# Kernel optimization log

Hardware: AMD Instinct MI355X
Metric: run time of the kernel (lower is better)

Reference implementation:

```python
import jax, jax.numpy as jnp
import numpy as np

N_NODES = 50000
N_EDGES = 800000
IN_FEATS = 128
HIDDEN = 128
OUT_LEN = 128


def setup_inputs() -> dict:
    key = jax.random.key(0)
    ks = jax.random.split(key, 8)
    feat = jax.random.normal(ks[0], (N_NODES, IN_FEATS), dtype=jnp.float32)
    # Glorot-ish init for weights, zeros for bias (DGL GraphConv default)
    def w(k, fi, fo):
        return jax.random.normal(k, (fi, fo), dtype=jnp.float32) / np.sqrt(fi)
    W1 = w(ks[1], IN_FEATS, HIDDEN)
    W2 = w(ks[2], HIDDEN, HIDDEN)
    W3 = w(ks[3], HIDDEN, OUT_LEN)
    b1 = jnp.zeros((HIDDEN,), jnp.float32)
    b2 = jnp.zeros((HIDDEN,), jnp.float32)
    b3 = jnp.zeros((OUT_LEN,), jnp.float32)
    src = jax.random.randint(ks[4], (N_EDGES,), 0, N_NODES, dtype=jnp.int32)
    dst = jax.random.randint(ks[5], (N_EDGES,), 0, N_NODES, dtype=jnp.int32)
    return {"feat": feat, "W1": W1, "b1": b1, "W2": W2, "b2": b2,
            "W3": W3, "b3": b3, "src": src, "dst": dst}


def _degree_norm(idx, n):
    # degree counts, clamped to min 1 (DGL behavior), then ^{-1/2}
    deg = jax.ops.segment_sum(jnp.ones_like(idx, dtype=jnp.float32), idx,
                              num_segments=n)
    return jax.lax.rsqrt(jnp.maximum(deg, 1.0))


def _graph_conv(x, W, b, src, dst, out_norm, in_norm):
    # DGL GraphConv, norm='both':
    # h = D_dst^{-1/2} * segsum_dst( D_src^{-1/2} * x[src] ) @ W + b
    h = x * out_norm[:, None]
    m = jax.ops.segment_sum(h[src], dst, num_segments=x.shape[0])  # [N, d]
    m = m * in_norm[:, None]
    return m @ W + b


def reference(feat, W1, b1, W2, b2, W3, b3, src, dst):
    out_norm = _degree_norm(src, feat.shape[0])  # out-degree norm (source)
    in_norm = _degree_norm(dst, feat.shape[0])   # in-degree norm (dest)
    h = jax.nn.relu(_graph_conv(feat, W1, b1, src, dst, out_norm, in_norm))
    h = jax.nn.relu(_graph_conv(h, W2, b2, src, dst, out_norm, in_norm))
    h = _graph_conv(h, W3, b3, src, dst, out_norm, in_norm)
    # single graph: mean_nodes == mean over all nodes, then squeeze -> [out_len]
    return jnp.mean(h, axis=0)
```

## Files before the change

### kernel.cpp

```cpp
#include <hip/hip_runtime.h>

#define N_NODES 50000
#define N_EDGES 800000
#define F 128
#define SCAN_NB 49
#define RN_NB 196
#define CH 64
#define EPC (N_EDGES / CH)
#define HALF 25000
#define QTR 12500
#define BSTRIDE 17
#define AGG_NB (N_NODES / 4)
#define GB ((N_NODES + 63) / 64)

typedef __bf16 bf16x8 __attribute__((ext_vector_type(8)));
typedef float  f32x4  __attribute__((ext_vector_type(4)));
typedef float  f32x2  __attribute__((ext_vector_type(2)));

__device__ inline unsigned short f2bf(float f) {
    unsigned u = __float_as_uint(f);
    u += 0x7FFF + ((u >> 16) & 1);
    return (unsigned short)(u >> 16);
}
__device__ inline unsigned packbf2(float a, float b) {
    return (unsigned)f2bf(a) | ((unsigned)f2bf(b) << 16);
}

__device__ inline void fp8x8_to_f32(uint2 u, float* f) {
    f32x2 v0 = __builtin_amdgcn_cvt_pk_f32_fp8(u.x, false);
    f32x2 v1 = __builtin_amdgcn_cvt_pk_f32_fp8(u.x, true);
    f32x2 v2 = __builtin_amdgcn_cvt_pk_f32_fp8(u.y, false);
    f32x2 v3 = __builtin_amdgcn_cvt_pk_f32_fp8(u.y, true);
    f[0] = v0.x; f[1] = v0.y; f[2] = v1.x; f[3] = v1.y;
    f[4] = v2.x; f[5] = v2.y; f[6] = v3.x; f[7] = v3.y;
}
__device__ inline unsigned f32x4_to_fp8(float a, float b, float c, float d) {
    unsigned r = __builtin_amdgcn_cvt_pk_fp8_f32(a, b, 0, false);
    r = __builtin_amdgcn_cvt_pk_fp8_f32(c, d, r, true);
    return r;
}

__global__ __launch_bounds__(1024) void hist_kernel(const int* __restrict__ src,
                                                    const int* __restrict__ dst,
                                                    unsigned short* __restrict__ Hs16,
                                                    unsigned short* __restrict__ Hd16) {
    __shared__ unsigned hist[HALF / 2];
    int bx = blockIdx.x;
    int c = bx >> 2, t = bx & 1, h = (bx >> 1) & 1;
    const int* ids = t ? dst : src;
    unsigned short* H = t ? Hd16 : Hs16;
    int base = h * HALF;
    for (int j = threadIdx.x; j < HALF / 2; j += 1024) hist[j] = 0;
    __syncthreads();
    int e0 = c * EPC;
    for (int e = e0 + threadIdx.x; e < e0 + EPC; e += 1024) {
        int id = ids[e] - base;
        if ((unsigned)id < (unsigned)HALF)
            atomicAdd(&hist[id >> 1], 1u << ((id & 1) * 16));
    }
    __syncthreads();
    for (int j = threadIdx.x; j < HALF / 2; j += 1024)
        *(unsigned*)&H[(size_t)c * N_NODES + base + 2 * j] = hist[j];
}

__global__ __launch_bounds__(256) void reduceN_kernel(const unsigned short* __restrict__ Hs16,
                                                      const unsigned short* __restrict__ Hd16,
                                                      float* __restrict__ onorm,
                                                      float* __restrict__ inorm,
                                                      int* __restrict__ degd,
                                                      int* __restrict__ bsums) {
    __shared__ int wsum[4];
    int i = blockIdx.x * 256 + threadIdx.x;
    int dd = 0;
    if (i < N_NODES) {
        int ds = 0;
        for (int c = 0; c < CH; c++) {
            ds += Hs16[(size_t)c * N_NODES + i];
            dd += Hd16[(size_t)c * N_NODES + i];
        }
        onorm[i] = rsqrtf(fmaxf((float)ds, 1.0f));
        inorm[i] = rsqrtf(fmaxf((float)dd, 1.0f));
        degd[i] = dd;
    }
    int v = dd;
#pragma unroll
    for (int off = 32; off; off >>= 1) v += __shfl_down(v, off);
    if ((threadIdx.x & 63) == 0) wsum[threadIdx.x >> 6] = v;
    __syncthreads();
    if (threadIdx.x == 0)
        bsums[blockIdx.x] = wsum[0] + wsum[1] + wsum[2] + wsum[3];
}

__global__ __launch_bounds__(1024) void tq_kernel(const int* __restrict__ src,
                                                  const int* __restrict__ dst,
                                                  const float* __restrict__ inorm,
                                                  float* __restrict__ Tq,
                                                  const float* __restrict__ feat,
                                                  const float* __restrict__ onorm,
                                                  uint2* __restrict__ xq,
                                                  const float* __restrict__ W1,
                                                  const float* __restrict__ W2,
                                                  unsigned short* __restrict__ Wt) {
    __shared__ float a[QTR];
    int bx = blockIdx.x;
    int c = bx >> 2, q = bx & 3;
    int base = q * QTR;
    for (int j = threadIdx.x; j < QTR; j += 1024) a[j] = 0.0f;
    __syncthreads();
    int e0 = c * EPC;
    for (int e = e0 + threadIdx.x; e < e0 + EPC; e += 1024) {
        int s = src[e] - base;
        if ((unsigned)s < (unsigned)QTR)
            atomicAdd(&a[s], inorm[dst[e]]);
    }
    __syncthreads();
    for (int j = threadIdx.x; j < QTR; j += 1024)
        Tq[(size_t)c * N_NODES + base + j] = a[j];

    int T = gridDim.x * 1024;
    int id0 = bx * 1024 + threadIdx.x;
    for (int i = id0; i < N_NODES * F / 8; i += T) {
        float w = onorm[i >> 4];
        const float4* xv = (const float4*)feat;
        float4 v0 = xv[i * 2], v1 = xv[i * 2 + 1];
        uint2 o;
        o.x = f32x4_to_fp8(v0.x * w, v0.y * w, v0.z * w, v0.w * w);
        o.y = f32x4_to_fp8(v1.x * w, v1.y * w, v1.z * w, v1.w * w);
        xq[i] = o;
    }
    for (int i = id0; i < 2 * F * F; i += T) {
        int wi = i >> 14, rem = i & 16383;
        int n = rem >> 7, k = rem & 127;
        const float* W = wi ? W2 : W1;
        Wt[(size_t)wi * F * F + (size_t)n * F + k] = f2bf(W[k * F + n]);
    }
}

__global__ __launch_bounds__(1024) void scanC_kernel(const int* __restrict__ deg,
                                                     const int* __restrict__ bsums,
                                                     int* __restrict__ rowst,
                                                     const unsigned short* __restrict__ Hd16,
                                                     int* __restrict__ P,
                                                     const float* __restrict__ Tq,
                                                     float* __restrict__ qt) {
    __shared__ int wsum[16];
    int t = threadIdx.x, lane = t & 63, w = t >> 6;
    int i = blockIdx.x * 1024 + t;
    int v = (i < N_NODES) ? deg[i] : 0;
    int incl = v;
#pragma unroll
    for (int off = 1; off < 64; off <<= 1) {
        int u = __shfl_up(incl, off);
        if (lane >= off) incl += u;
    }
    if (lane == 63) wsum[w] = incl;
    __syncthreads();
    if (t == 0) {
        int s = 0;
        int kmax = min(4 * (int)blockIdx.x, RN_NB);
        for (int k = 0; k < kmax; k++) s += bsums[k];
#pragma unroll
        for (int k = 0; k < 16; k++) { int x = wsum[k]; wsum[k] = s; s += x; }
    }
    __syncthreads();
    incl += wsum[w];
    if (i < N_NODES) {
        int s = incl - v;
        rowst[i] = s;
        if (i == N_NODES - 1) rowst[N_NODES] = incl;
        float tsum = 0.0f;
        for (int c = 0; c < CH; c++) {
            size_t o = (size_t)c * N_NODES + i;
            P[o] = s; s += Hd16[o];
            tsum += Tq[o];
        }
        qt[i] = tsum;
    }
}

__global__ __launch_bounds__(1024) void scatter2_kernel(const int* __restrict__ src,
                                                        const int* __restrict__ dst,
                                                        const int* __restrict__ P,
                                                        int* __restrict__ esrc) {
    __shared__ int cur[QTR];
    int bx = blockIdx.x;
    int c = bx >> 2, q = bx & 3;
    int base = q * QTR;
    for (int j = threadIdx.x; j < QTR; j += 1024)
        cur[j] = P[(size_t)c * N_NODES + base + j];
    __syncthreads();
    int e0 = c * EPC;
    for (int e = e0 + threadIdx.x; e < e0 + EPC; e += 1024) {
        int d = dst[e] - base;
        if ((unsigned)d < (unsigned)QTR) {
            int pos = atomicAdd(&cur[d], 1);
            esrc[pos] = src[e];
        }
    }
}

__global__ __launch_bounds__(256) void agg_csr_kernel(const uint2* __restrict__ xq,
                                                      uint4* __restrict__ mb,
                                                      const int* __restrict__ rowst,
                                                      const int* __restrict__ esrc,
                                                      const float* __restrict__ inorm) {
    int w = threadIdx.x >> 6;
    int lane = threadIdx.x & 63;
    int g = lane >> 4, t = lane & 15;
    int row = blockIdx.x * 4 + w;
    int beg = __builtin_amdgcn_readfirstlane(rowst[row]);
    int end = __builtin_amdgcn_readfirstlane(rowst[row + 1]);
    float acc[8];
#pragma unroll
    for (int k = 0; k < 8; k++) acc[k] = 0.0f;

    for (int e = beg; e < end; e += 16) {
        int ea = min(e + g,      end - 1);
        int eb = min(e + 4 + g,  end - 1);
        int ec = min(e + 8 + g,  end - 1);
        int ed = min(e + 12 + g, end - 1);
        int sa = esrc[ea], sb = esrc[eb], sc = esrc[ec], sd = esrc[ed];
        uint2 ua = xq[(size_t)sa * 16 + t];
        uint2 ub = xq[(size_t)sb * 16 + t];
        uint2 uc = xq[(size_t)sc * 16 + t];
        uint2 ud = xq[(size_t)sd * 16 + t];
        float wa = (e + g      < end) ? 1.0f : 0.0f;
        float wb = (e + 4 + g  < end) ? 1.0f : 0.0f;
        float wc = (e + 8 + g  < end) ? 1.0f : 0.0f;
        float wd = (e + 12 + g < end) ? 1.0f : 0.0f;
        float fa[8], fb[8], fc[8], fd[8];
        fp8x8_to_f32(ua, fa); fp8x8_to_f32(ub, fb);
        fp8x8_to_f32(uc, fc); fp8x8_to_f32(ud, fd);
#pragma unroll
        for (int k = 0; k < 8; k++)
            acc[k] += fa[k] * wa + fb[k] * wb + fc[k] * wc + fd[k] * wd;
    }
#pragma unroll
    for (int k = 0; k < 8; k++) {
        acc[k] += __shfl_xor(acc[k], 16, 64);
        acc[k] += __shfl_xor(acc[k], 32, 64);
    }
    if (g == 0) {
        float inw = inorm[row];
        uint4 o;
        o.x = packbf2(acc[0] * inw, acc[1] * inw);
        o.y = packbf2(acc[2] * inw, acc[3] * inw);
        o.z = packbf2(acc[4] * inw, acc[5] * inw);
        o.w = packbf2(acc[6] * inw, acc[7] * inw);
        mb[(size_t)row * 16 + t] = o;
    }
}

template <int FINAL>
__global__ __launch_bounds__(256) void mfma_gemm_kernel(const unsigned short* __restrict__ A,
                                                        const unsigned short* __restrict__ Wt,
                                                        const float* __restrict__ bias,
                                                        const float* __restrict__ onorm,
                                                        unsigned char* __restrict__ Y8,
                                                        const float* __restrict__ qt,
                                                        float* __restrict__ part2) {
    __shared__ uint4 sB[F * BSTRIDE];
    __shared__ float sPf[4][F];
    int tid = threadIdx.x;
    int w = tid >> 6;
    int lane = tid & 63;
    int quad = lane >> 4, r16 = lane & 15;
    int row0 = blockIdx.x * 64 + w * 16;

    const uint4* Arow = (const uint4*)(A + (size_t)(row0 + r16) * F);
    uint4 a[4];
#pragma unroll
    for (int kk = 0; kk < 4; kk++) a[kk] = Arow[kk * 4 + quad];

    const uint4* G = (const uint4*)Wt;
    for (int j = tid; j < F * 16; j += 256)
        sB[(j >> 4) * BSTRIDE + (j & 15)] = G[j];

    f32x4 acc[8];
#pragma unroll
    for (int t = 0; t < 8; t++) acc[t] = (f32x4){0.f, 0.f, 0.f, 0.f};
    __syncthreads();

#pragma unroll
    for (int kk = 0; kk < 4; kk++) {
        bf16x8 av = __builtin_bit_cast(bf16x8, a[kk]);
#pragma unroll
        for (int t = 0; t < 8; t++) {
            bf16x8 bv = __builtin_bit_cast(bf16x8,
                sB[(t * 16 + r16) * BSTRIDE + kk * 4 + quad]);
            acc[t] = __builtin_amdgcn_mfma_f32_16x16x32_bf16(av, bv, acc[t], 0, 0, 0);
        }
    }

    float rw[4];
#pragma unroll
    for (int reg = 0; reg < 4; reg++) {
        int row = row0 + quad * 4 + reg;
        rw[reg] = (row < N_NODES) ? (FINAL ? qt[row] * onorm[row] : onorm[row]) : 0.0f;
    }

    if (!FINAL) {
#pragma unroll
        for (int t = 0; t < 8; t++) {
            int col = t * 16 + r16;
            float bb = bias[col];
#pragma unroll
            for (int reg = 0; reg < 4; reg++) {
                int row = row0 + quad * 4 + reg;
                if (row < N_NODES) {
                    float v = fmaxf(acc[t][reg] + bb, 0.0f) * rw[reg];
                    unsigned p = __builtin_amdgcn_cvt_pk_fp8_f32(v, v, 0, false);
                    Y8[(size_t)row * F + col] = (unsigned char)(p & 0xFF);
                }
            }
        }
    } else {
#pragma unroll
        for (int t = 0; t < 8; t++) {
            int col = t * 16 + r16;
            float bb = bias[col];
            float p = 0.0f;
#pragma unroll
            for (int reg = 0; reg < 4; reg++)
                p += fmaxf(acc[t][reg] + bb, 0.0f) * rw[reg];
            p += __shfl_xor(p, 16, 64);
            p += __shfl_xor(p, 32, 64);
            if (quad == 0) sPf[w][col] = p;
        }
        __syncthreads();
        if (tid < F)
            part2[(size_t)blockIdx.x * F + tid] =
                sPf[0][tid] + sPf[1][tid] + sPf[2][tid] + sPf[3][tid];
    }
}

__global__ __launch_bounds__(1024) void final_kernel(const float* __restrict__ part2,
                                                     const float* __restrict__ W3,
                                                     const float* __restrict__ b3,
                                                     float* __restrict__ out) {
    __shared__ float sc[8][F];
    int tid = threadIdx.x;
    int col = tid & 127, sl = tid >> 7;
    float acc = 0.0f;
    for (int b = sl; b < GB; b += 8) acc += part2[(size_t)b * F + col];
    sc[sl][col] = acc;
    __syncthreads();
    if (tid < F) {
        float s = 0.0f;
#pragma unroll
        for (int k = 0; k < 8; k++) s += sc[k][tid];
        sc[0][tid] = s * (1.0f / (float)N_NODES);
    }
    __syncthreads();
    if (tid < F) {
        float o = b3[tid];
        for (int k = 0; k < F; k++) o += sc[0][k] * W3[k * F + tid];
        out[tid] = o;
    }
}

extern "C" void kernel_launch(void* const* d_in, const int* in_sizes, int n_in,
                              void* d_out, int out_size, void* d_ws, size_t ws_size,
                              hipStream_t stream) {
    const float* feat = (const float*)d_in[0];
    const float* W1   = (const float*)d_in[1];
    const float* b1   = (const float*)d_in[2];
    const float* W2   = (const float*)d_in[3];
    const float* b2   = (const float*)d_in[4];
    const float* W3   = (const float*)d_in[5];
    const float* b3   = (const float*)d_in[6];
    const int*   src  = (const int*)d_in[7];
    const int*   dst  = (const int*)d_in[8];
    float* out = (float*)d_out;

    char* ws = (char*)d_ws;
    size_t off = 0;
    uint4* mb    = (uint4*)(ws + off); off += (size_t)N_NODES * F * 2;
    float* Tq    = (float*)(ws + off); off += (size_t)CH * N_NODES * 4;
    int*   P     = (int*)  (ws + off); off += (size_t)CH * N_NODES * 4;
    unsigned short* Hs16 = (unsigned short*)(ws + off); off += (size_t)CH * N_NODES * 2;
    unsigned short* Hd16 = (unsigned short*)(ws + off); off += (size_t)CH * N_NODES * 2;
    uint2* xq    = (uint2*)(ws + off); off += (size_t)N_NODES * F;
    uint2* hq    = (uint2*)(ws + off); off += (size_t)N_NODES * F;
    unsigned short* Wt = (unsigned short*)(ws + off); off += 2 * F * F * 2;
    float* part2 = (float*)(ws + off); off += (size_t)GB * F * 4;
    int*   esrc  = (int*)  (ws + off); off += (size_t)N_EDGES * 4;
    float* onorm = (float*)(ws + off); off += N_NODES * 4;
    float* inorm = (float*)(ws + off); off += N_NODES * 4;
    float* qt    = (float*)(ws + off); off += N_NODES * 4;
    int*   degd  = (int*)  (ws + off); off += N_NODES * 4;
    int*   rowst = (int*)  (ws + off); off += (N_NODES + 1) * 4;
    int*   bsums = (int*)  (ws + off); off += 256 * 4;

    hist_kernel<<<4 * CH, 1024, 0, stream>>>(src, dst, Hs16, Hd16);
    reduceN_kernel<<<RN_NB, 256, 0, stream>>>(Hs16, Hd16, onorm, inorm, degd, bsums);
    tq_kernel<<<4 * CH, 1024, 0, stream>>>(src, dst, inorm, Tq,
                                           feat, onorm, xq, W1, W2, Wt);
    scanC_kernel<<<SCAN_NB, 1024, 0, stream>>>(degd, bsums, rowst, Hd16, P, Tq, qt);
    scatter2_kernel<<<4 * CH, 1024, 0, stream>>>(src, dst, P, esrc);

    agg_csr_kernel<<<AGG_NB, 256, 0, stream>>>(xq, mb, rowst, esrc, inorm);
    mfma_gemm_kernel<0><<<GB, 256, 0, stream>>>((const unsigned short*)mb, Wt, b1,
                                                onorm, (unsigned char*)hq, qt, part2);
    agg_csr_kernel<<<AGG_NB, 256, 0, stream>>>(hq, mb, rowst, esrc, inorm);
    mfma_gemm_kernel<1><<<GB, 256, 0, stream>>>((const unsigned short*)mb, Wt + F * F,
                                                b2, onorm, (unsigned char*)hq, qt, part2);
    final_kernel<<<1, 1024, 0, stream>>>(part2, W3, b3, out);
}
```

Baseline: 233.0 us.

## Fuse CSR aggregation into MFMA GEMM kernel via shared-memory A tile

Merges the gather-aggregation kernel and the bf16 MFMA GEMM into one kernel. Each wave aggregates 16 destination rows one after another and stores the bf16 results in a shared-memory A tile, which the GEMM then consumes directly. This removes the intermediate mb buffer's global write and read and two kernel launches. In exchange, each wave now handles rows serially instead of one row per wave across many blocks, and the extra shared memory lowers occupancy. Both changes can cut the memory-level parallelism the latency-bound gather depends on.

Result: slower. 308.5 us (+32.4%).

```diff
diff --git a/kernel.cpp b/kernel.cpp
--- a/kernel.cpp
+++ b/kernel.cpp
@@ -10,7 +10,6 @@
 #define HALF 25000
 #define QTR 12500
 #define BSTRIDE 17
-#define AGG_NB (N_NODES / 4)
 #define GB ((N_NODES + 63) / 64)
 
 typedef __bf16 bf16x8 __attribute__((ext_vector_type(8)));
@@ -199,116 +198,110 @@
     }
 }
 
-__global__ __launch_bounds__(256) void agg_csr_kernel(const uint2* __restrict__ xq,
-                                                      uint4* __restrict__ mb,
-                                                      const int* __restrict__ rowst,
-                                                      const int* __restrict__ esrc,
-                                                      const float* __restrict__ inorm) {
-    int w = threadIdx.x >> 6;
-    int lane = threadIdx.x & 63;
-    int g = lane >> 4, t = lane & 15;
-    int row = blockIdx.x * 4 + w;
-    int beg = __builtin_amdgcn_readfirstlane(rowst[row]);
-    int end = __builtin_amdgcn_readfirstlane(rowst[row + 1]);
-    float acc[8];
-#pragma unroll
-    for (int k = 0; k < 8; k++) acc[k] = 0.0f;
-
-    for (int e = beg; e < end; e += 16) {
-        int ea = min(e + g,      end - 1);
-        int eb = min(e + 4 + g,  end - 1);
-        int ec = min(e + 8 + g,  end - 1);
-        int ed = min(e + 12 + g, end - 1);
-        int sa = esrc[ea], sb = esrc[eb], sc = esrc[ec], sd = esrc[ed];
-        uint2 ua = xq[(size_t)sa * 16 + t];
-        uint2 ub = xq[(size_t)sb * 16 + t];
-        uint2 uc = xq[(size_t)sc * 16 + t];
-        uint2 ud = xq[(size_t)sd * 16 + t];
-        float wa = (e + g      < end) ? 1.0f : 0.0f;
-        float wb = (e + 4 + g  < end) ? 1.0f : 0.0f;
-        float wc = (e + 8 + g  < end) ? 1.0f : 0.0f;
-        float wd = (e + 12 + g < end) ? 1.0f : 0.0f;
-        float fa[8], fb[8], fc[8], fd[8];
-        fp8x8_to_f32(ua, fa); fp8x8_to_f32(ub, fb);
-        fp8x8_to_f32(uc, fc); fp8x8_to_f32(ud, fd);
-#pragma unroll
-        for (int k = 0; k < 8; k++)
-            acc[k] += fa[k] * wa + fb[k] * wb + fc[k] * wc + fd[k] * wd;
-    }
-#pragma unroll
-    for (int k = 0; k < 8; k++) {
-        acc[k] += __shfl_xor(acc[k], 16, 64);
-        acc[k] += __shfl_xor(acc[k], 32, 64);
-    }
-    if (g == 0) {
-        float inw = inorm[row];
-        uint4 o;
-        o.x = packbf2(acc[0] * inw, acc[1] * inw);
-        o.y = packbf2(acc[2] * inw, acc[3] * inw);
-        o.z = packbf2(acc[4] * inw, acc[5] * inw);
-        o.w = packbf2(acc[6] * inw, acc[7] * inw);
-        mb[(size_t)row * 16 + t] = o;
-    }
-}
-
 template <int FINAL>
-__global__ __launch_bounds__(256) void mfma_gemm_kernel(const unsigned short* __restrict__ A,
-                                                        const unsigned short* __restrict__ Wt,
-                                                        const float* __restrict__ bias,
-                                                        const float* __restrict__ onorm,
-                                                        unsigned char* __restrict__ Y8,
-                                                        const float* __restrict__ qt,
-                                                        float* __restrict__ part2) {
+__global__ __launch_bounds__(256) void agg_gemm_kernel(const uint2* __restrict__ xq,
+                                                       const int* __restrict__ rowst,
+                                                       const int* __restrict__ esrc,
+                                                       const float* __restrict__ inorm,
+                                                       const unsigned short* __restrict__ Wt,
+                                                       const float* __restrict__ bias,
+                                                       const float* __restrict__ onorm,
+                                                       unsigned char* __restrict__ Y8,
+                                                       const float* __restrict__ qt,
+                                                       float* __restrict__ part2) {
     __shared__ uint4 sB[F * BSTRIDE];
+    __shared__ uint4 sA[64 * BSTRIDE];
     __shared__ float sPf[4][F];
     int tid = threadIdx.x;
     int w = tid >> 6;
     int lane = tid & 63;
     int quad = lane >> 4, r16 = lane & 15;
-    int row0 = blockIdx.x * 64 + w * 16;
-
-    const uint4* Arow = (const uint4*)(A + (size_t)(row0 + r16) * F);
-    uint4 a[4];
-#pragma unroll
-    for (int kk = 0; kk < 4; kk++) a[kk] = Arow[kk * 4 + quad];
+    int g = quad, t = r16;
+    int row0 = blockIdx.x * 64;
+    int rw0 = row0 + w * 16;
 
     const uint4* G = (const uint4*)Wt;
     for (int j = tid; j < F * 16; j += 256)
         sB[(j >> 4) * BSTRIDE + (j & 15)] = G[j];
 
+    for (int r = 0; r < 16; r++) {
+        int row = rw0 + r;
+        uint4 o = {0u, 0u, 0u, 0u};
+        if (row < N_NODES) {
+            int beg = __builtin_amdgcn_readfirstlane(rowst[row]);
+            int end = __builtin_amdgcn_readfirstlane(rowst[row + 1]);
+            float acc[8];
+#pragma unroll
+            for (int k = 0; k < 8; k++) acc[k] = 0.0f;
+            for (int e = beg; e < end; e += 16) {
+                int ea = min(e + g,      end - 1);
+                int eb = min(e + 4 + g,  end - 1);
+                int ec = min(e + 8 + g,  end - 1);
+                int ed = min(e + 12 + g, end - 1);
+                int sa = esrc[ea], sb = esrc[eb], sc = esrc[ec], sd = esrc[ed];
+                uint2 ua = xq[(size_t)sa * 16 + t];
+                uint2 ub = xq[(size_t)sb * 16 + t];
+                uint2 uc = xq[(size_t)sc * 16 + t];
+                uint2 ud = xq[(size_t)sd * 16 + t];
+                float wa = (e + g      < end) ? 1.0f : 0.0f;
+                float wb = (e + 4 + g  < end) ? 1.0f : 0.0f;
+                float wc = (e + 8 + g  < end) ? 1.0f : 0.0f;
+                float wd = (e + 12 + g < end) ? 1.0f : 0.0f;
+                float fa[8], fb[8], fc[8], fd[8];
+                fp8x8_to_f32(ua, fa); fp8x8_to_f32(ub, fb);
+                fp8x8_to_f32(uc, fc); fp8x8_to_f32(ud, fd);
+#pragma unroll
+                for (int k = 0; k < 8; k++)
+                    acc[k] += fa[k] * wa + fb[k] * wb + fc[k] * wc + fd[k] * wd;
+            }
+#pragma unroll
+            for (int k = 0; k < 8; k++) {
+                acc[k] += __shfl_xor(acc[k], 16, 64);
+                acc[k] += __shfl_xor(acc[k], 32, 64);
+            }
+            float inw = inorm[row];
+            o.x = packbf2(acc[0] * inw, acc[1] * inw);
+            o.y = packbf2(acc[2] * inw, acc[3] * inw);
+            o.z = packbf2(acc[4] * inw, acc[5] * inw);
+            o.w = packbf2(acc[6] * inw, acc[7] * inw);
+        }
+        if (g == 0) sA[(w * 16 + r) * BSTRIDE + t] = o;
+    }
+
     f32x4 acc[8];
 #pragma unroll
-    for (int t = 0; t < 8; t++) acc[t] = (f32x4){0.f, 0.f, 0.f, 0.f};
+    for (int n = 0; n < 8; n++) acc[n] = (f32x4){0.f, 0.f, 0.f, 0.f};
     __syncthreads();
 
 #pragma unroll
     for (int kk = 0; kk < 4; kk++) {
-        bf16x8 av = __builtin_bit_cast(bf16x8, a[kk]);
-#pragma unroll
-        for (int t = 0; t < 8; t++) {
+        bf16x8 av = __builtin_bit_cast(bf16x8,
+            sA[(w * 16 + r16) * BSTRIDE + kk * 4 + quad]);
+#pragma unroll
+        for (int n = 0; n < 8; n++) {
             bf16x8 bv = __builtin_bit_cast(bf16x8,
-                sB[(t * 16 + r16) * BSTRIDE + kk * 4 + quad]);
-            acc[t] = __builtin_amdgcn_mfma_f32_16x16x32_bf16(av, bv, acc[t], 0, 0, 0);
+                sB[(n * 16 + r16) * BSTRIDE + kk * 4 + quad]);
+            acc[n] = __builtin_amdgcn_mfma_f32_16x16x32_bf16(av, bv, acc[n], 0, 0, 0);
         }
     }
 
     float rw[4];
 #pragma unroll
     for (int reg = 0; reg < 4; reg++) {
-        int row = row0 + quad * 4 + reg;
+        int row = rw0 + quad * 4 + reg;
         rw[reg] = (row < N_NODES) ? (FINAL ? qt[row] * onorm[row] : onorm[row]) : 0.0f;
     }
 
     if (!FINAL) {
 #pragma unroll
-        for (int t = 0; t < 8; t++) {
-            int col = t * 16 + r16;
+        for (int n = 0; n < 8; n++) {
+            int col = n * 16 + r16;
             float bb = bias[col];
 #pragma unroll
             for (int reg = 0; reg < 4; reg++) {
-                int row = row0 + quad * 4 + reg;
+                int row = rw0 + quad * 4 + reg;
                 if (row < N_NODES) {
-                    float v = fmaxf(acc[t][reg] + bb, 0.0f) * rw[reg];
+                    float v = fmaxf(acc[n][reg] + bb, 0.0f) * rw[reg];
                     unsigned p = __builtin_amdgcn_cvt_pk_fp8_f32(v, v, 0, false);
                     Y8[(size_t)row * F + col] = (unsigned char)(p & 0xFF);
                 }
@@ -316,13 +309,13 @@
         }
     } else {
 #pragma unroll
-        for (int t = 0; t < 8; t++) {
-            int col = t * 16 + r16;
+        for (int n = 0; n < 8; n++) {
+            int col = n * 16 + r16;
             float bb = bias[col];
             float p = 0.0f;
 #pragma unroll
             for (int reg = 0; reg < 4; reg++)
-                p += fmaxf(acc[t][reg] + bb, 0.0f) * rw[reg];
+                p += fmaxf(acc[n][reg] + bb, 0.0f) * rw[reg];
             p += __shfl_xor(p, 16, 64);
             p += __shfl_xor(p, 32, 64);
             if (quad == 0) sPf[w][col] = p;
@@ -375,7 +368,6 @@
 
     char* ws = (char*)d_ws;
     size_t off = 0;
-    uint4* mb    = (uint4*)(ws + off); off += (size_t)N_NODES * F * 2;
     float* Tq    = (float*)(ws + off); off += (size_t)CH * N_NODES * 4;
     int*   P     = (int*)  (ws + off); off += (size_t)CH * N_NODES * 4;
     unsigned short* Hs16 = (unsigned short*)(ws + off); off += (size_t)CH * N_NODES * 2;
@@ -399,11 +391,9 @@
     scanC_kernel<<<SCAN_NB, 1024, 0, stream>>>(degd, bsums, rowst, Hd16, P, Tq, qt);
     scatter2_kernel<<<4 * CH, 1024, 0, stream>>>(src, dst, P, esrc);
 
-    agg_csr_kernel<<<AGG_NB, 256, 0, stream>>>(xq, mb, rowst, esrc, inorm);
-    mfma_gemm_kernel<0><<<GB, 256, 0, stream>>>((const unsigned short*)mb, Wt, b1,
-                                                onorm, (unsigned char*)hq, qt, part2);
-    agg_csr_kernel<<<AGG_NB, 256, 0, stream>>>(hq, mb, rowst, esrc, inorm);
-    mfma_gemm_kernel<1><<<GB, 256, 0, stream>>>((const unsigned short*)mb, Wt + F * F,
-                                                b2, onorm, (unsigned char*)hq, qt, part2);
+    agg_gemm_kernel<0><<<GB, 256, 0, stream>>>(xq, rowst, esrc, inorm, Wt, b1,
+                                               onorm, (unsigned char*)hq, qt, part2);
+    agg_gemm_kernel<1><<<GB, 256, 0, stream>>>(hq, rowst, esrc, inorm, Wt + F * F, b2,
+                                               onorm, (unsigned char*)hq, qt, part2);
     final_kernel<<<1, 1024, 0, stream>>>(part2, W3, b3, out);
 }
```

## Merge graph-preprocessing kernels into one cooperative kernel with grid syncs

Applied to the files above, without the earlier changes.

Replaces five separate preprocessing launches (histogram, degree reduce, Tq/quantize, scan, scatter) with a single cooperative kernel of 256 blocks of 1024 threads that separates the phases with grid.sync(). The goal is to remove the launch gaps and tail drain between the small phases. The degree-reduce step now runs on 49 blocks of 1024 threads instead of 196 blocks of 256, and the scan sums per-block totals accordingly. The risks are lower parallelism in those phases, the cost of each grid barrier, and the requirement that all 256 blocks be co-resident.

After: 381.7 us. +63.8%, slower.

```diff
diff --git a/kernel.cpp b/kernel.cpp
--- a/kernel.cpp
+++ b/kernel.cpp
@@ -1,10 +1,12 @@
 #include <hip/hip_runtime.h>
+#include <hip/hip_cooperative_groups.h>
+
+namespace cg = cooperative_groups;
 
 #define N_NODES 50000
 #define N_EDGES 800000
 #define F 128
 #define SCAN_NB 49
-#define RN_NB 196
 #define CH 64
 #define EPC (N_EDGES / CH)
 #define HALF 25000
@@ -40,161 +42,154 @@
     return r;
 }
 
-__global__ __launch_bounds__(1024) void hist_kernel(const int* __restrict__ src,
-                                                    const int* __restrict__ dst,
-                                                    unsigned short* __restrict__ Hs16,
-                                                    unsigned short* __restrict__ Hd16) {
-    __shared__ unsigned hist[HALF / 2];
+__global__ __launch_bounds__(1024) void build_kernel(
+        const int* __restrict__ src, const int* __restrict__ dst,
+        unsigned short* __restrict__ Hs16, unsigned short* __restrict__ Hd16,
+        float* __restrict__ onorm, float* __restrict__ inorm,
+        int* __restrict__ degd, int* __restrict__ bsums,
+        const float* __restrict__ feat, uint2* __restrict__ xq,
+        const float* __restrict__ W1, const float* __restrict__ W2,
+        unsigned short* __restrict__ Wt,
+        float* __restrict__ Tq, int* __restrict__ rowst,
+        int* __restrict__ P, float* __restrict__ qt,
+        int* __restrict__ esrc) {
+    cg::grid_group grid = cg::this_grid();
+    __shared__ __align__(16) unsigned ubuf[QTR];
+    __shared__ int wsum[16];
     int bx = blockIdx.x;
-    int c = bx >> 2, t = bx & 1, h = (bx >> 1) & 1;
-    const int* ids = t ? dst : src;
-    unsigned short* H = t ? Hd16 : Hs16;
-    int base = h * HALF;
-    for (int j = threadIdx.x; j < HALF / 2; j += 1024) hist[j] = 0;
-    __syncthreads();
-    int e0 = c * EPC;
-    for (int e = e0 + threadIdx.x; e < e0 + EPC; e += 1024) {
-        int id = ids[e] - base;
-        if ((unsigned)id < (unsigned)HALF)
-            atomicAdd(&hist[id >> 1], 1u << ((id & 1) * 16));
-    }
-    __syncthreads();
-    for (int j = threadIdx.x; j < HALF / 2; j += 1024)
-        *(unsigned*)&H[(size_t)c * N_NODES + base + 2 * j] = hist[j];
-}
-
-__global__ __launch_bounds__(256) void reduceN_kernel(const unsigned short* __restrict__ Hs16,
-                                                      const unsigned short* __restrict__ Hd16,
-                                                      float* __restrict__ onorm,
-                                                      float* __restrict__ inorm,
-                                                      int* __restrict__ degd,
-                                                      int* __restrict__ bsums) {
-    __shared__ int wsum[4];
-    int i = blockIdx.x * 256 + threadIdx.x;
-    int dd = 0;
-    if (i < N_NODES) {
-        int ds = 0;
-        for (int c = 0; c < CH; c++) {
-            ds += Hs16[(size_t)c * N_NODES + i];
-            dd += Hd16[(size_t)c * N_NODES + i];
-        }
-        onorm[i] = rsqrtf(fmaxf((float)ds, 1.0f));
-        inorm[i] = rsqrtf(fmaxf((float)dd, 1.0f));
-        degd[i] = dd;
-    }
-    int v = dd;
-#pragma unroll
-    for (int off = 32; off; off >>= 1) v += __shfl_down(v, off);
-    if ((threadIdx.x & 63) == 0) wsum[threadIdx.x >> 6] = v;
-    __syncthreads();
-    if (threadIdx.x == 0)
-        bsums[blockIdx.x] = wsum[0] + wsum[1] + wsum[2] + wsum[3];
-}
-
-__global__ __launch_bounds__(1024) void tq_kernel(const int* __restrict__ src,
-                                                  const int* __restrict__ dst,
-                                                  const float* __restrict__ inorm,
-                                                  float* __restrict__ Tq,
-                                                  const float* __restrict__ feat,
-                                                  const float* __restrict__ onorm,
-                                                  uint2* __restrict__ xq,
-                                                  const float* __restrict__ W1,
-                                                  const float* __restrict__ W2,
-                                                  unsigned short* __restrict__ Wt) {
-    __shared__ float a[QTR];
-    int bx = blockIdx.x;
-    int c = bx >> 2, q = bx & 3;
-    int base = q * QTR;
-    for (int j = threadIdx.x; j < QTR; j += 1024) a[j] = 0.0f;
-    __syncthreads();
-    int e0 = c * EPC;
-    for (int e = e0 + threadIdx.x; e < e0 + EPC; e += 1024) {
-        int s = src[e] - base;
-        if ((unsigned)s < (unsigned)QTR)
-            atomicAdd(&a[s], inorm[dst[e]]);
-    }
-    __syncthreads();
-    for (int j = threadIdx.x; j < QTR; j += 1024)
-        Tq[(size_t)c * N_NODES + base + j] = a[j];
-
-    int T = gridDim.x * 1024;
-    int id0 = bx * 1024 + threadIdx.x;
-    for (int i = id0; i < N_NODES * F / 8; i += T) {
-        float w = onorm[i >> 4];
-        const float4* xv = (const float4*)feat;
-        float4 v0 = xv[i * 2], v1 = xv[i * 2 + 1];
-        uint2 o;
-        o.x = f32x4_to_fp8(v0.x * w, v0.y * w, v0.z * w, v0.w * w);
-        o.y = f32x4_to_fp8(v1.x * w, v1.y * w, v1.z * w, v1.w * w);
-        xq[i] = o;
-    }
-    for (int i = id0; i < 2 * F * F; i += T) {
-        int wi = i >> 14, rem = i & 16383;
-        int n = rem >> 7, k = rem & 127;
-        const float* W = wi ? W2 : W1;
-        Wt[(size_t)wi * F * F + (size_t)n * F + k] = f2bf(W[k * F + n]);
-    }
-}
-
-__global__ __launch_bounds__(1024) void scanC_kernel(const int* __restrict__ deg,
-                                                     const int* __restrict__ bsums,
-                                                     int* __restrict__ rowst,
-                                                     const unsigned short* __restrict__ Hd16,
-                                                     int* __restrict__ P,
-                                                     const float* __restrict__ Tq,
-                                                     float* __restrict__ qt) {
-    __shared__ int wsum[16];
-    int t = threadIdx.x, lane = t & 63, w = t >> 6;
-    int i = blockIdx.x * 1024 + t;
-    int v = (i < N_NODES) ? deg[i] : 0;
-    int incl = v;
-#pragma unroll
-    for (int off = 1; off < 64; off <<= 1) {
-        int u = __shfl_up(incl, off);
-        if (lane >= off) incl += u;
-    }
-    if (lane == 63) wsum[w] = incl;
-    __syncthreads();
-    if (t == 0) {
-        int s = 0;
-        int kmax = min(4 * (int)blockIdx.x, RN_NB);
-        for (int k = 0; k < kmax; k++) s += bsums[k];
-#pragma unroll
-        for (int k = 0; k < 16; k++) { int x = wsum[k]; wsum[k] = s; s += x; }
-    }
-    __syncthreads();
-    incl += wsum[w];
-    if (i < N_NODES) {
-        int s = incl - v;
-        rowst[i] = s;
-        if (i == N_NODES - 1) rowst[N_NODES] = incl;
-        float tsum = 0.0f;
-        for (int c = 0; c < CH; c++) {
-            size_t o = (size_t)c * N_NODES + i;
-            P[o] = s; s += Hd16[o];
-            tsum += Tq[o];
-        }
-        qt[i] = tsum;
-    }
-}
-
-__global__ __launch_bounds__(1024) void scatter2_kernel(const int* __restrict__ src,
-                                                        const int* __restrict__ dst,
-                                                        const int* __restrict__ P,
-                                                        int* __restrict__ esrc) {
-    __shared__ int cur[QTR];
-    int bx = blockIdx.x;
-    int c = bx >> 2, q = bx & 3;
-    int base = q * QTR;
-    for (int j = threadIdx.x; j < QTR; j += 1024)
-        cur[j] = P[(size_t)c * N_NODES + base + j];
-    __syncthreads();
-    int e0 = c * EPC;
-    for (int e = e0 + threadIdx.x; e < e0 + EPC; e += 1024) {
-        int d = dst[e] - base;
-        if ((unsigned)d < (unsigned)QTR) {
-            int pos = atomicAdd(&cur[d], 1);
-            esrc[pos] = src[e];
+    int tid = threadIdx.x;
+
+    {
+        int c = bx >> 2, t = bx & 1, h = (bx >> 1) & 1;
+        const int* ids = t ? dst : src;
+        unsigned short* H = t ? Hd16 : Hs16;
+        int base = h * HALF;
+        for (int j = tid; j < HALF / 2; j += 1024) ubuf[j] = 0;
+        __syncthreads();
+        int e0 = c * EPC;
+        for (int e = e0 + tid; e < e0 + EPC; e += 1024) {
+            int id = ids[e] - base;
+            if ((unsigned)id < (unsigned)HALF)
+                atomicAdd(&ubuf[id >> 1], 1u << ((id & 1) * 16));
+        }
+        __syncthreads();
+        for (int j = tid; j < HALF / 2; j += 1024)
+            *(unsigned*)&H[(size_t)c * N_NODES + base + 2 * j] = ubuf[j];
+    }
+    grid.sync();
+
+    if (bx < SCAN_NB) {
+        int i = bx * 1024 + tid;
+        int dd = 0;
+        if (i < N_NODES) {
+            int ds = 0;
+            for (int c = 0; c < CH; c++) {
+                ds += Hs16[(size_t)c * N_NODES + i];
+                dd += Hd16[(size_t)c * N_NODES + i];
+            }
+            onorm[i] = rsqrtf(fmaxf((float)ds, 1.0f));
+            inorm[i] = rsqrtf(fmaxf((float)dd, 1.0f));
+            degd[i] = dd;
+        }
+        int v = dd;
+#pragma unroll
+        for (int off = 32; off; off >>= 1) v += __shfl_down(v, off);
+        if ((tid & 63) == 0) wsum[tid >> 6] = v;
+        __syncthreads();
+        if (tid == 0) {
+            int s = 0;
+#pragma unroll
+            for (int k = 0; k < 16; k++) s += wsum[k];
+            bsums[bx] = s;
+        }
+    }
+    grid.sync();
+
+    {
+        float* a = (float*)ubuf;
+        int c = bx >> 2, q = bx & 3;
+        int base = q * QTR;
+        for (int j = tid; j < QTR; j += 1024) a[j] = 0.0f;
+        __syncthreads();
+        int e0 = c * EPC;
+        for (int e = e0 + tid; e < e0 + EPC; e += 1024) {
+            int s = src[e] - base;
+            if ((unsigned)s < (unsigned)QTR)
+                atomicAdd(&a[s], inorm[dst[e]]);
+        }
+        __syncthreads();
+        for (int j = tid; j < QTR; j += 1024)
+            Tq[(size_t)c * N_NODES + base + j] = a[j];
+
+        int T = gridDim.x * 1024;
+        int id0 = bx * 1024 + tid;
+        for (int i = id0; i < N_NODES * F / 8; i += T) {
+            float w = onorm[i >> 4];
+            const float4* xv = (const float4*)feat;
+            float4 v0 = xv[i * 2], v1 = xv[i * 2 + 1];
+            uint2 o;
+            o.x = f32x4_to_fp8(v0.x * w, v0.y * w, v0.z * w, v0.w * w);
+            o.y = f32x4_to_fp8(v1.x * w, v1.y * w, v1.z * w, v1.w * w);
+            xq[i] = o;
+        }
+        for (int i = id0; i < 2 * F * F; i += T) {
+            int wi = i >> 14, rem = i & 16383;
+            int n = rem >> 7, k = rem & 127;
+            const float* W = wi ? W2 : W1;
+            Wt[(size_t)wi * F * F + (size_t)n * F + k] = f2bf(W[k * F + n]);
+        }
+    }
+    grid.sync();
+
+    if (bx < SCAN_NB) {
+        int t = tid, lane = t & 63, w = t >> 6;
+        int i = bx * 1024 + t;
+        int v = (i < N_NODES) ? degd[i] : 0;
+        int incl = v;
+#pragma unroll
+        for (int off = 1; off < 64; off <<= 1) {
+            int u = __shfl_up(incl, off);
+            if (lane >= off) incl += u;
+        }
+        if (lane == 63) wsum[w] = incl;
+        __syncthreads();
+        if (t == 0) {
+            int s = 0;
+            for (int k = 0; k < bx; k++) s += bsums[k];
+#pragma unroll
+            for (int k = 0; k < 16; k++) { int x = wsum[k]; wsum[k] = s; s += x; }
+        }
+        __syncthreads();
+        incl += wsum[w];
+        if (i < N_NODES) {
+            int s = incl - v;
+            rowst[i] = s;
+            if (i == N_NODES - 1) rowst[N_NODES] = incl;
+            float tsum = 0.0f;
+            for (int c = 0; c < CH; c++) {
+                size_t o = (size_t)c * N_NODES + i;
+                P[o] = s; s += Hd16[o];
+                tsum += Tq[o];
+            }
+            qt[i] = tsum;
+        }
+    }
+    grid.sync();
+
+    {
+        int* cur = (int*)ubuf;
+        int c = bx >> 2, q = bx & 3;
+        int base = q * QTR;
+        for (int j = tid; j < QTR; j += 1024)
+            cur[j] = P[(size_t)c * N_NODES + base + j];
+        __syncthreads();
+        int e0 = c * EPC;
+        for (int e = e0 + tid; e < e0 + EPC; e += 1024) {
+            int d = dst[e] - base;
+            if ((unsigned)d < (unsigned)QTR) {
+                int pos = atomicAdd(&cur[d], 1);
+                esrc[pos] = src[e];
+            }
         }
     }
 }
@@ -389,15 +384,18 @@
     float* inorm = (float*)(ws + off); off += N_NODES * 4;
     float* qt    = (float*)(ws + off); off += N_NODES * 4;
     int*   degd  = (int*)  (ws + off); off += N_NODES * 4;
-    int*   rowst = (int*)  (ws + off); off += (N_NODES + 1) * 4;
-    int*   bsums = (int*)  (ws + off); off += 256 * 4;
-
-    hist_kernel<<<4 * CH, 1024, 0, stream>>>(src, dst, Hs16, Hd16);
-    reduceN_kernel<<<RN_NB, 256, 0, stream>>>(Hs16, Hd16, onorm, inorm, degd, bsums);
-    tq_kernel<<<4 * CH, 1024, 0, stream>>>(src, dst, inorm, Tq,
-                                           feat, onorm, xq, W1, W2, Wt);
-    scanC_kernel<<<SCAN_NB, 1024, 0, stream>>>(degd, bsums, rowst, Hd16, P, Tq, qt);
-    scatter2_kernel<<<4 * CH, 1024, 0, stream>>>(src, dst, P, esrc);
+    int*   rowst = (int*)(ws + off); off += (N_NODES + 1) * 4;
+    int*   bsums = (int*)(ws + off); off += 256 * 4;
+
+    {
+        void* args[] = {(void*)&src, (void*)&dst, (void*)&Hs16, (void*)&Hd16,
+                        (void*)&onorm, (void*)&inorm, (void*)&degd, (void*)&bsums,
+                        (void*)&feat, (void*)&xq, (void*)&W1, (void*)&W2,
+                        (void*)&Wt, (void*)&Tq, (void*)&rowst, (void*)&P,
+                        (void*)&qt, (void*)&esrc};
+        hipLaunchCooperativeKernel((const void*)build_kernel, dim3(4 * CH),
+                                   dim3(1024), args, 0, stream);
+    }
 
     agg_csr_kernel<<<AGG_NB, 256, 0, stream>>>(xq, mb, rowst, esrc, inorm);
     mfma_gemm_kernel<0><<<GB, 256, 0, stream>>>((const unsigned short*)mb, Wt, b1,
```

## Replace chunked LDS histogram CSR build with global atomic degree and scatter

Applied to the files above, without the earlier changes.

Drops the 64-chunk shared-memory histograms, per-chunk prefix tables and the separate scatter pass. Degrees, the qt accumulation and CSR edge placement now use global atomics directly over vectorized int4 edge reads, with a simpler scan and an init kernel that zeroes buffers and transposes the weights. This removes large intermediate buffers (Hs16, Hd16, Tq, P) and the repeated edge passes, at the cost of contended global atomics and a nondeterministic edge order within rows. The GEMM row index is also clamped to avoid out-of-bounds reads on the last tile.

New measurement: 331.1 us. +42.1%, slower.

```diff
diff --git a/kernel.cpp b/kernel.cpp
--- a/kernel.cpp
+++ b/kernel.cpp
@@ -3,12 +3,8 @@
 #define N_NODES 50000
 #define N_EDGES 800000
 #define F 128
+#define RN_NB 196
 #define SCAN_NB 49
-#define RN_NB 196
-#define CH 64
-#define EPC (N_EDGES / CH)
-#define HALF 25000
-#define QTR 12500
 #define BSTRIDE 17
 #define AGG_NB (N_NODES / 4)
 #define GB ((N_NODES + 63) / 64)
@@ -40,47 +36,52 @@
     return r;
 }
 
-__global__ __launch_bounds__(1024) void hist_kernel(const int* __restrict__ src,
-                                                    const int* __restrict__ dst,
-                                                    unsigned short* __restrict__ Hs16,
-                                                    unsigned short* __restrict__ Hd16) {
-    __shared__ unsigned hist[HALF / 2];
-    int bx = blockIdx.x;
-    int c = bx >> 2, t = bx & 1, h = (bx >> 1) & 1;
-    const int* ids = t ? dst : src;
-    unsigned short* H = t ? Hd16 : Hs16;
-    int base = h * HALF;
-    for (int j = threadIdx.x; j < HALF / 2; j += 1024) hist[j] = 0;
-    __syncthreads();
-    int e0 = c * EPC;
-    for (int e = e0 + threadIdx.x; e < e0 + EPC; e += 1024) {
-        int id = ids[e] - base;
-        if ((unsigned)id < (unsigned)HALF)
-            atomicAdd(&hist[id >> 1], 1u << ((id & 1) * 16));
-    }
-    __syncthreads();
-    for (int j = threadIdx.x; j < HALF / 2; j += 1024)
-        *(unsigned*)&H[(size_t)c * N_NODES + base + 2 * j] = hist[j];
-}
-
-__global__ __launch_bounds__(256) void reduceN_kernel(const unsigned short* __restrict__ Hs16,
-                                                      const unsigned short* __restrict__ Hd16,
-                                                      float* __restrict__ onorm,
-                                                      float* __restrict__ inorm,
-                                                      int* __restrict__ degd,
-                                                      int* __restrict__ bsums) {
+__global__ __launch_bounds__(256) void init_kernel(int* __restrict__ degS,
+                                                   int* __restrict__ degD,
+                                                   float* __restrict__ qtacc,
+                                                   const float* __restrict__ W1,
+                                                   const float* __restrict__ W2,
+                                                   unsigned short* __restrict__ Wt) {
+    int T = gridDim.x * 256;
+    int id0 = blockIdx.x * 256 + threadIdx.x;
+    for (int i = id0; i < N_NODES; i += T) {
+        degS[i] = 0; degD[i] = 0; qtacc[i] = 0.0f;
+    }
+    for (int i = id0; i < 2 * F * F; i += T) {
+        int wi = i >> 14, rem = i & 16383;
+        int n = rem >> 7, k = rem & 127;
+        const float* W = wi ? W2 : W1;
+        Wt[(size_t)wi * F * F + (size_t)n * F + k] = f2bf(W[k * F + n]);
+    }
+}
+
+__global__ __launch_bounds__(1024) void deg_kernel(const int4* __restrict__ src4,
+                                                   const int4* __restrict__ dst4,
+                                                   int* __restrict__ degS,
+                                                   int* __restrict__ degD) {
+    int T = gridDim.x * 1024;
+    for (int i = blockIdx.x * 1024 + threadIdx.x; i < N_EDGES / 4; i += T) {
+        int4 s = src4[i], d = dst4[i];
+        atomicAdd(&degS[s.x], 1); atomicAdd(&degS[s.y], 1);
+        atomicAdd(&degS[s.z], 1); atomicAdd(&degS[s.w], 1);
+        atomicAdd(&degD[d.x], 1); atomicAdd(&degD[d.y], 1);
+        atomicAdd(&degD[d.z], 1); atomicAdd(&degD[d.w], 1);
+    }
+}
+
+__global__ __launch_bounds__(256) void norms_kernel(const int* __restrict__ degS,
+                                                    const int* __restrict__ degD,
+                                                    float* __restrict__ onorm,
+                                                    float* __restrict__ inorm,
+                                                    int* __restrict__ bsums) {
     __shared__ int wsum[4];
     int i = blockIdx.x * 256 + threadIdx.x;
     int dd = 0;
     if (i < N_NODES) {
-        int ds = 0;
-        for (int c = 0; c < CH; c++) {
-            ds += Hs16[(size_t)c * N_NODES + i];
-            dd += Hd16[(size_t)c * N_NODES + i];
-        }
+        int ds = degS[i];
+        dd = degD[i];
         onorm[i] = rsqrtf(fmaxf((float)ds, 1.0f));
         inorm[i] = rsqrtf(fmaxf((float)dd, 1.0f));
-        degd[i] = dd;
     }
     int v = dd;
 #pragma unroll
@@ -91,34 +92,68 @@
         bsums[blockIdx.x] = wsum[0] + wsum[1] + wsum[2] + wsum[3];
 }
 
-__global__ __launch_bounds__(1024) void tq_kernel(const int* __restrict__ src,
-                                                  const int* __restrict__ dst,
-                                                  const float* __restrict__ inorm,
-                                                  float* __restrict__ Tq,
-                                                  const float* __restrict__ feat,
-                                                  const float* __restrict__ onorm,
-                                                  uint2* __restrict__ xq,
-                                                  const float* __restrict__ W1,
-                                                  const float* __restrict__ W2,
-                                                  unsigned short* __restrict__ Wt) {
-    __shared__ float a[QTR];
-    int bx = blockIdx.x;
-    int c = bx >> 2, q = bx & 3;
-    int base = q * QTR;
-    for (int j = threadIdx.x; j < QTR; j += 1024) a[j] = 0.0f;
-    __syncthreads();
-    int e0 = c * EPC;
-    for (int e = e0 + threadIdx.x; e < e0 + EPC; e += 1024) {
-        int s = src[e] - base;
-        if ((unsigned)s < (unsigned)QTR)
-            atomicAdd(&a[s], inorm[dst[e]]);
-    }
-    __syncthreads();
-    for (int j = threadIdx.x; j < QTR; j += 1024)
-        Tq[(size_t)c * N_NODES + base + j] = a[j];
-
+__global__ __launch_bounds__(1024) void scan_kernel(const int* __restrict__ degD,
+                                                    const int* __restrict__ bsums,
+                                                    int* __restrict__ rowst,
+                                                    int* __restrict__ cur) {
+    __shared__ int wsum[16];
+    __shared__ int sbase;
+    int t = threadIdx.x, lane = t & 63, w = t >> 6;
+    int i = blockIdx.x * 1024 + t;
+    int v = (i < N_NODES) ? degD[i] : 0;
+    int incl = v;
+#pragma unroll
+    for (int off = 1; off < 64; off <<= 1) {
+        int u = __shfl_up(incl, off);
+        if (lane >= off) incl += u;
+    }
+    if (lane == 63) wsum[w] = incl;
+    int kmax = min(4 * (int)blockIdx.x, RN_NB);
+    if (t < 64) {
+        int s = 0;
+        for (int k = t; k < kmax; k += 64) s += bsums[k];
+#pragma unroll
+        for (int off = 32; off; off >>= 1) s += __shfl_down(s, off);
+        if (t == 0) sbase = s;
+    }
+    __syncthreads();
+    if (t == 0) {
+        int s = sbase;
+#pragma unroll
+        for (int k = 0; k < 16; k++) { int x = wsum[k]; wsum[k] = s; s += x; }
+    }
+    __syncthreads();
+    incl += wsum[w];
+    if (i < N_NODES) {
+        int s = incl - v;
+        rowst[i] = s;
+        cur[i] = s;
+        if (i == N_NODES - 1) rowst[N_NODES] = incl;
+    }
+}
+
+__global__ __launch_bounds__(1024) void edge_kernel(const int4* __restrict__ src4,
+                                                    const int4* __restrict__ dst4,
+                                                    const float* __restrict__ inorm,
+                                                    float* __restrict__ qtacc,
+                                                    int* __restrict__ cur,
+                                                    int* __restrict__ esrc,
+                                                    const float* __restrict__ feat,
+                                                    const float* __restrict__ onorm,
+                                                    uint2* __restrict__ xq) {
     int T = gridDim.x * 1024;
-    int id0 = bx * 1024 + threadIdx.x;
+    int id0 = blockIdx.x * 1024 + threadIdx.x;
+    for (int i = id0; i < N_EDGES / 4; i += T) {
+        int4 s = src4[i], d = dst4[i];
+#pragma unroll
+        for (int k = 0; k < 4; k++) {
+            int sv = (k == 0) ? s.x : (k == 1) ? s.y : (k == 2) ? s.z : s.w;
+            int dv = (k == 0) ? d.x : (k == 1) ? d.y : (k == 2) ? d.z : d.w;
+            atomicAdd(&qtacc[sv], inorm[dv]);
+            int pos = atomicAdd(&cur[dv], 1);
+            esrc[pos] = sv;
+        }
+    }
     for (int i = id0; i < N_NODES * F / 8; i += T) {
         float w = onorm[i >> 4];
         const float4* xv = (const float4*)feat;
@@ -127,75 +162,6 @@
         o.x = f32x4_to_fp8(v0.x * w, v0.y * w, v0.z * w, v0.w * w);
         o.y = f32x4_to_fp8(v1.x * w, v1.y * w, v1.z * w, v1.w * w);
         xq[i] = o;
-    }
-    for (int i = id0; i < 2 * F * F; i += T) {
-        int wi = i >> 14, rem = i & 16383;
-        int n = rem >> 7, k = rem & 127;
-        const float* W = wi ? W2 : W1;
-        Wt[(size_t)wi * F * F + (size_t)n * F + k] = f2bf(W[k * F + n]);
-    }
-}
-
-__global__ __launch_bounds__(1024) void scanC_kernel(const int* __restrict__ deg,
-                                                     const int* __restrict__ bsums,
-                                                     int* __restrict__ rowst,
-                                                     const unsigned short* __restrict__ Hd16,
-                                                     int* __restrict__ P,
-                                                     const float* __restrict__ Tq,
-                                                     float* __restrict__ qt) {
-    __shared__ int wsum[16];
-    int t = threadIdx.x, lane = t & 63, w = t >> 6;
-    int i = blockIdx.x * 1024 + t;
-    int v = (i < N_NODES) ? deg[i] : 0;
-    int incl = v;
-#pragma unroll
-    for (int off = 1; off < 64; off <<= 1) {
-        int u = __shfl_up(incl, off);
-        if (lane >= off) incl += u;
-    }
-    if (lane == 63) wsum[w] = incl;
-    __syncthreads();
-    if (t == 0) {
-        int s = 0;
-        int kmax = min(4 * (int)blockIdx.x, RN_NB);
-        for (int k = 0; k < kmax; k++) s += bsums[k];
-#pragma unroll
-        for (int k = 0; k < 16; k++) { int x = wsum[k]; wsum[k] = s; s += x; }
-    }
-    __syncthreads();
-    incl += wsum[w];
-    if (i < N_NODES) {
-        int s = incl - v;
-        rowst[i] = s;
-        if (i == N_NODES - 1) rowst[N_NODES] = incl;
-        float tsum = 0.0f;
-        for (int c = 0; c < CH; c++) {
-            size_t o = (size_t)c * N_NODES + i;
-            P[o] = s; s += Hd16[o];
-            tsum += Tq[o];
-        }
-        qt[i] = tsum;
-    }
-}
-
-__global__ __launch_bounds__(1024) void scatter2_kernel(const int* __restrict__ src,
-                                                        const int* __restrict__ dst,
-                                                        const int* __restrict__ P,
-                                                        int* __restrict__ esrc) {
-    __shared__ int cur[QTR];
-    int bx = blockIdx.x;
-    int c = bx >> 2, q = bx & 3;
-    int base = q * QTR;
-    for (int j = threadIdx.x; j < QTR; j += 1024)
-        cur[j] = P[(size_t)c * N_NODES + base + j];
-    __syncthreads();
-    int e0 = c * EPC;
-    for (int e = e0 + threadIdx.x; e < e0 + EPC; e += 1024) {
-        int d = dst[e] - base;
-        if ((unsigned)d < (unsigned)QTR) {
-            int pos = atomicAdd(&cur[d], 1);
-            esrc[pos] = src[e];
-        }
     }
 }
 
@@ -267,7 +233,8 @@
     int quad = lane >> 4, r16 = lane & 15;
     int row0 = blockIdx.x * 64 + w * 16;
 
-    const uint4* Arow = (const uint4*)(A + (size_t)(row0 + r16) * F);
+    int arow = min(row0 + r16, N_NODES - 1);
+    const uint4* Arow = (const uint4*)(A + (size_t)arow * F);
     uint4 a[4];
 #pragma unroll
     for (int kk = 0; kk < 4; kk++) a[kk] = Arow[kk * 4 + quad];
@@ -376,34 +343,35 @@
     char* ws = (char*)d_ws;
     size_t off = 0;
     uint4* mb    = (uint4*)(ws + off); off += (size_t)N_NODES * F * 2;
-    float* Tq    = (float*)(ws + off); off += (size_t)CH * N_NODES * 4;
-    int*   P     = (int*)  (ws + off); off += (size_t)CH * N_NODES * 4;
-    unsigned short* Hs16 = (unsigned short*)(ws + off); off += (size_t)CH * N_NODES * 2;
-    unsigned short* Hd16 = (unsigned short*)(ws + off); off += (size_t)CH * N_NODES * 2;
     uint2* xq    = (uint2*)(ws + off); off += (size_t)N_NODES * F;
     uint2* hq    = (uint2*)(ws + off); off += (size_t)N_NODES * F;
+    int*   esrc  = (int*)  (ws + off); off += (size_t)N_EDGES * 4;
     unsigned short* Wt = (unsigned short*)(ws + off); off += 2 * F * F * 2;
     float* part2 = (float*)(ws + off); off += (size_t)GB * F * 4;
-    int*   esrc  = (int*)  (ws + off); off += (size_t)N_EDGES * 4;
     float* onorm = (float*)(ws + off); off += N_NODES * 4;
     float* inorm = (float*)(ws + off); off += N_NODES * 4;
-    float* qt    = (float*)(ws + off); off += N_NODES * 4;
-    int*   degd  = (int*)  (ws + off); off += N_NODES * 4;
+    float* qtacc = (float*)(ws + off); off += N_NODES * 4;
+    int*   degS  = (int*)  (ws + off); off += N_NODES * 4;
+    int*   degD  = (int*)  (ws + off); off += N_NODES * 4;
+    int*   cur   = (int*)  (ws + off); off += N_NODES * 4;
     int*   rowst = (int*)  (ws + off); off += (N_NODES + 1) * 4;
     int*   bsums = (int*)  (ws + off); off += 256 * 4;
 
-    hist_kernel<<<4 * CH, 1024, 0, stream>>>(src, dst, Hs16, Hd16);
-    reduceN_kernel<<<RN_NB, 256, 0, stream>>>(Hs16, Hd16, onorm, inorm, degd, bsums);
-    tq_kernel<<<4 * CH, 1024, 0, stream>>>(src, dst, inorm, Tq,
-                                           feat, onorm, xq, W1, W2, Wt);
-    scanC_kernel<<<SCAN_NB, 1024, 0, stream>>>(degd, bsums, rowst, Hd16, P, Tq, qt);
-    scatter2_kernel<<<4 * CH, 1024, 0, stream>>>(src, dst, P, esrc);
+    const int4* src4 = (const int4*)src;
+    const int4* dst4 = (const int4*)dst;
+
+    init_kernel<<<256, 256, 0, stream>>>(degS, degD, qtacc, W1, W2, Wt);
+    deg_kernel<<<196, 1024, 0, stream>>>(src4, dst4, degS, degD);
+    norms_kernel<<<RN_NB, 256, 0, stream>>>(degS, degD, onorm, inorm, bsums);
+    scan_kernel<<<SCAN_NB, 1024, 0, stream>>>(degD, bsums, rowst, cur);
+    edge_kernel<<<256, 1024, 0, stream>>>(src4, dst4, inorm, qtacc, cur, esrc,
+                                          feat, onorm, xq);
 
     agg_csr_kernel<<<AGG_NB, 256, 0, stream>>>(xq, mb, rowst, esrc, inorm);
     mfma_gemm_kernel<0><<<GB, 256, 0, stream>>>((const unsigned short*)mb, Wt, b1,
-                                                onorm, (unsigned char*)hq, qt, part2);
+                                                onorm, (unsigned char*)hq, qtacc, part2);
     agg_csr_kernel<<<AGG_NB, 256, 0, stream>>>(hq, mb, rowst, esrc, inorm);
     mfma_gemm_kernel<1><<<GB, 256, 0, stream>>>((const unsigned short*)mb, Wt + F * F,
-                                                b2, onorm, (unsigned char*)hq, qt, part2);
+                                                b2, onorm, (unsigned char*)hq, qtacc, part2);
     final_kernel<<<1, 1024, 0, stream>>>(part2, W3, b3, out);
 }
```
